# Optimization experiments

Measured on AMD Instinct MI355X. Metric: run time of the kernel, lower is better.

The kernel has to match this reference:

```python
import jax, jax.numpy as jnp
from jax import lax
import numpy as np

DIM = 512; DEPTH = 2; DSTATE = 16; EXPAND = 4; NEXP = 4
DIN = DIM * EXPAND; DTRANK = (DIM + 15) // 16; DCONV = 4; HID = DIM * EXPAND
BATCH = 2; SEQ = 2048; CAP_FACTOR = 1.0; EPS = 1e-6


def setup_inputs():
    key = jax.random.key(0)
    ks = jax.random.split(key, 12)
    f = lambda k, s: jax.random.normal(k, s, jnp.float32) * 0.02
    return {
        "x": jax.random.normal(ks[0], (BATCH, SEQ, DIM), jnp.float32),
        "in_w": f(ks[1], (DEPTH, 2 * DIN, DIM)),
        "conv_w": f(ks[2], (DEPTH, DIN, 1, DCONV)),
        "conv_b": jnp.zeros((DEPTH, DIN), jnp.float32),
        "xproj_w": f(ks[3], (DEPTH, DTRANK + 2 * DSTATE, DIN)),
        "dt_w": f(ks[4], (DEPTH, DIN, DTRANK)),
        "dt_b": jnp.zeros((DEPTH, DIN), jnp.float32),
        "A_log": jnp.tile(jnp.log(jnp.arange(1, DSTATE + 1, dtype=jnp.float32))[None, None, :], (DEPTH, DIN, 1)),
        "Dp": jnp.ones((DEPTH, DIN), jnp.float32),
        "out_w": f(ks[5], (DEPTH, DIM, DIN)),
        "gate_w": f(ks[6], (DEPTH, NEXP, DIM)),
        "gate_b": jnp.zeros((DEPTH, NEXP), jnp.float32),
        "w1": f(ks[7], (DEPTH, NEXP, HID, DIM)),
        "b1": jnp.zeros((DEPTH, NEXP, HID), jnp.float32),
        "w2": f(ks[8], (DEPTH, NEXP, DIM, HID)),
        "b2": jnp.zeros((DEPTH, NEXP, DIM), jnp.float32),
    }


def _switch_moe(x, gw, gb, w1, b1, w2, b2):
    # zeta SwitchGate: softmax -> top-1 mask -> normalize by batch-dim sum, scale by capacity
    gs = jax.nn.softmax(jnp.einsum('bld,ed->ble', x, gw) + gb, axis=-1)  # (b,l,E)
    mask = jax.nn.one_hot(jnp.argmax(gs, axis=-1), NEXP, dtype=gs.dtype)
    masked = gs * mask
    capacity = int(CAP_FACTOR * x.shape[0])
    gate = masked / (masked.sum(axis=0, keepdims=True) + EPS) * capacity  # (b,l,E)
    # zeta SwitchMoE runs every expert on every token, then gate-weighted sum
    h = jax.nn.gelu(jnp.einsum('bld,ehd->bleh', x, w1) + b1, approximate=False)  # (b,l,E,HID)
    eo = jnp.einsum('bleh,edh->bled', h, w2) + b2                                 # (b,l,E,d)
    return jnp.einsum('bled,ble->bld', eo, gate)


def _mamba(x, in_w, conv_w, conv_b, xproj_w, dt_w, dt_b, A_log, Dp, out_w):
    b, l, d = x.shape
    xz = jnp.einsum('bld,ed->ble', x, in_w)   # (b,l,2*DIN)
    u, res = xz[..., :DIN], xz[..., DIN:]
    # causal depthwise conv: torch pads both sides by DCONV-1 then crops to L == left-pad only
    uc = lax.conv_general_dilated(u.transpose(0, 2, 1), conv_w, (1,), [(DCONV - 1, 0)],
                                  feature_group_count=DIN,
                                  dimension_numbers=('NCH', 'OIH', 'NCH'))
    u = jax.nn.silu((uc + conv_b[None, :, None]).transpose(0, 2, 1))  # (b,l,DIN)
    dbc = jnp.einsum('bld,ed->ble', u, xproj_w)                       # (b,l,DTRANK+2n)
    delta = jax.nn.softplus(jnp.einsum('blr,dr->bld', dbc[..., :DTRANK], dt_w) + dt_b)  # (b,l,DIN)
    B = dbc[..., DTRANK:DTRANK + DSTATE]
    C = dbc[..., DTRANK + DSTATE:]
    A = -jnp.exp(A_log)                                               # (DIN,n)

    def step(s, t):
        dt, Bt, Ct, ut = t  # (b,DIN),(b,n),(b,n),(b,DIN)
        s = jnp.exp(dt[:, :, None] * A) * s + (dt * ut)[:, :, None] * Bt[:, None, :]
        return s, jnp.einsum('bdn,bn->bd', s, Ct)

    s0 = jnp.zeros((b, DIN, DSTATE), x.dtype)
    _, ys = lax.scan(step, s0, (delta.transpose(1, 0, 2), B.transpose(1, 0, 2),
                                C.transpose(1, 0, 2), u.transpose(1, 0, 2)))
    y = ys.transpose(1, 0, 2) + u * Dp
    y = y * jax.nn.silu(res)
    return jnp.einsum('ble,de->bld', y, out_w)


def reference(x, in_w, conv_w, conv_b, xproj_w, dt_w, dt_b, A_log, Dp, out_w,
              gate_w, gate_b, w1, b1, w2, b2):
    for i in range(DEPTH):
        x = _switch_moe(x, gate_w[i], gate_b[i], w1[i], b1[i], w2[i], b2[i])
        x = _mamba(x, in_w[i], conv_w[i], conv_b[i], xproj_w[i], dt_w[i], dt_b[i],
                   A_log[i], Dp[i], out_w[i]) + x
        x = _switch_moe(x, gate_w[i], gate_b[i], w1[i], b1[i], w2[i], b2[i])
    return x
```

## Files before the change

kernel.cpp:

```cpp
#include <hip/hip_runtime.h>
#include <math.h>
#include <stdint.h>

typedef unsigned short u16;
typedef __attribute__((ext_vector_type(8))) _Float16 f16x8;
typedef __attribute__((ext_vector_type(4))) float f32x4;
typedef __attribute__((ext_vector_type(4))) u16 u16x4;

constexpr int DIM_    = 512;
constexpr int NEXP_   = 4;
constexpr int DIN_    = 2048;
constexpr int DTRANK_ = 32;
constexpr int DSTATE_ = 16;
constexpr int HID_    = 2048;
constexpr int BATCH_  = 2;
constexpr int SEQ_    = 2048;
constexpr int NTOK_   = BATCH_ * SEQ_;
constexpr float EPS_  = 1e-6f;

constexpr int NCHUNK_ = 32;
constexpr int CLEN_   = SEQ_ / NCHUNK_;

__device__ __forceinline__ float siluf(float x)     { return x / (1.f + __expf(-x)); }
__device__ __forceinline__ float geluf(float x)     { return 0.5f * x * (1.f + erff(x * 0.70710678118654752440f)); }
__device__ __forceinline__ float softplusf(float x) { return x > 20.f ? x : log1pf(__expf(x)); }

__device__ __forceinline__ float h2f(u16 b) { return (float)__builtin_bit_cast(_Float16, b); }
__device__ __forceinline__ void fsplit(float v, u16& h, u16& l) {
    _Float16 hh = (_Float16)v;
    float r = v - (float)hh;
    _Float16 ll = (_Float16)r;
    h = __builtin_bit_cast(u16, hh);
    l = __builtin_bit_cast(u16, ll);
}

__device__ __forceinline__ void gload16(const void* g, void* l) {
    __builtin_amdgcn_global_load_lds(
        (const __attribute__((address_space(1))) unsigned*)(uintptr_t)g,
        (__attribute__((address_space(3))) unsigned*)(uintptr_t)l,
        16, 0, 0);
}

enum { EPI_NONE = 0, EPI_GELU = 1, EPI_SCALE_BIAS = 2, EPI_RESID = 4 };

template <int EPI, bool OUTF32, bool SPLITK = false>
__global__ __launch_bounds__(256, 2) void gemm_split(
    const u16* __restrict__ Ah, const u16* __restrict__ Al, int lda,
    const u16* __restrict__ Wh, const u16* __restrict__ Wl, int ldw, long wstride,
    const float* __restrict__ bias, int bstride,
    u16* __restrict__ Ch, u16* __restrict__ Cl, float* __restrict__ Cf, int ldc,
    int M, int K,
    const int* __restrict__ counts, const int* __restrict__ perm, int permstride,
    const float* __restrict__ scale,
    const u16* __restrict__ Rh, const u16* __restrict__ Rl, int ldr)
{
    const int nwg = gridDim.x * gridDim.y * gridDim.z;
    int lid = blockIdx.x + gridDim.x * (blockIdx.y + gridDim.y * blockIdx.z);
    {
        const int q = nwg >> 3, r = nwg & 7;
        const int xcd = lid & 7, idx = lid >> 3;
        lid = (xcd < r ? xcd * (q + 1) : r * (q + 1) + (xcd - r) * q) + idx;
    }
    const int bx = lid % gridDim.x;
    const int rest = lid / gridDim.x;
    const int by = rest % gridDim.y;
    const int bz = rest / gridDim.y;

    const int e  = (SPLITK || !counts) ? 0 : bz;
    const int Me = counts ? counts[e] : M;
    const int m0 = bx * 64;
    if (m0 >= Me) return;
    const int kbase = SPLITK ? bz * K : 0;
    const int n0 = by * 64;
    const int* rows = perm ? (perm + (long)e * permstride) : nullptr;
    const u16* Whe = Wh + (long)e * wstride;
    const u16* Wle = Wl + (long)e * wstride;
    const float* be = bias ? (bias + (long)e * bstride) : nullptr;
    float* Cfo = SPLITK ? (Cf + (size_t)bz * M * ldc) : Cf;

    __shared__ __attribute__((aligned(16))) u16 AsH[2][4096], AsL[2][4096];
    __shared__ __attribute__((aligned(16))) u16 BsH[2][4096], BsL[2][4096];

    const int tid  = threadIdx.x;
    const int lane = tid & 63;
    const int wave = tid >> 6;
    const int wr = wave >> 1, wc = wave & 1;

    const int slot = tid & 7;
    const int rloc = tid >> 3;
    const int eoff = ((slot ^ (rloc & 7)) << 3) + kbase;
    const int ldst = tid * 8;

    long asrc[2];
#pragma unroll
    for (int i = 0; i < 2; i++) {
        int gr = m0 + i * 32 + rloc;
        int src = rows ? rows[gr < Me ? gr : Me - 1] : gr;
        asrc[i] = (long)src * lda + eoff;
    }
    long bsrc[2];
#pragma unroll
    for (int i = 0; i < 2; i++)
        bsrc[i] = (long)(n0 + i * 32 + rloc) * ldw + eoff;

    auto stage = [&](int buf, int k0) {
#pragma unroll
        for (int i = 0; i < 2; i++) {
            gload16(Ah + asrc[i] + k0, &AsH[buf][i * 2048 + ldst]);
            gload16(Al + asrc[i] + k0, &AsL[buf][i * 2048 + ldst]);
            gload16(Whe + bsrc[i] + k0, &BsH[buf][i * 2048 + ldst]);
            gload16(Wle + bsrc[i] + k0, &BsL[buf][i * 2048 + ldst]);
        }
    };

    f32x4 zero = {0.f, 0.f, 0.f, 0.f};
    f32x4 acc[2][2];
#pragma unroll
    for (int m = 0; m < 2; m++)
#pragma unroll
        for (int n = 0; n < 2; n++) acc[m][n] = zero;

    const int lr = lane & 15;
    const int kq = (lane >> 4) * 8;

    const int NT = K / 64;
    stage(0, 0);
    __syncthreads();

    for (int t = 0; t < NT; ++t) {
        const int buf = t & 1;
        if (t + 1 < NT) stage(buf ^ 1, (t + 1) * 64);
#pragma unroll
        for (int kk = 0; kk < 2; kk++) {
            const int lk = kk * 32 + kq;
            f16x8 ah[2], al[2], bh[2], bl[2];
#pragma unroll
            for (int m = 0; m < 2; m++) {
                int row = wr * 32 + m * 16 + lr;
                int off = row * 64 + (lk ^ ((row & 7) << 3));
                ah[m] = *(const f16x8*)&AsH[buf][off];
                al[m] = *(const f16x8*)&AsL[buf][off];
            }
#pragma unroll
            for (int n = 0; n < 2; n++) {
                int row = wc * 32 + n * 16 + lr;
                int off = row * 64 + (lk ^ ((row & 7) << 3));
                bh[n] = *(const f16x8*)&BsH[buf][off];
                bl[n] = *(const f16x8*)&BsL[buf][off];
            }
#pragma unroll
            for (int m = 0; m < 2; m++)
#pragma unroll
                for (int n = 0; n < 2; n++) {
                    acc[m][n] = __builtin_amdgcn_mfma_f32_16x16x32_f16(ah[m], bh[n], acc[m][n], 0, 0, 0);
                    acc[m][n] = __builtin_amdgcn_mfma_f32_16x16x32_f16(ah[m], bl[n], acc[m][n], 0, 0, 0);
                    acc[m][n] = __builtin_amdgcn_mfma_f32_16x16x32_f16(al[m], bh[n], acc[m][n], 0, 0, 0);
                }
        }
        __syncthreads();
    }

    const int rq = lane >> 4;
#pragma unroll
    for (int m = 0; m < 2; m++) {
#pragma unroll
        for (int n = 0; n < 2; n++) {
            const int col = n0 + wc * 32 + n * 16 + lr;
            const float bv = be ? be[col] : 0.f;
#pragma unroll
            for (int r = 0; r < 4; r++) {
                const int gr = m0 + wr * 32 + m * 16 + rq * 4 + r;
                if (gr >= Me) continue;
                const long crow = rows ? rows[gr] : gr;
                float v = acc[m][n][r];
                if constexpr (EPI == EPI_GELU)            v = geluf(v + bv);
                else if constexpr (EPI == EPI_SCALE_BIAS) v = scale[crow] * (v + bv);
                else if constexpr (EPI == EPI_RESID)
                    v += h2f(Rh[crow * ldr + col]) + h2f(Rl[crow * ldr + col]);
                if constexpr (OUTF32) {
                    Cfo[crow * ldc + col] = v;
                } else {
                    u16 hh, ll; fsplit(v, hh, ll);
                    Ch[crow * ldc + col] = hh;
                    Cl[crow * ldc + col] = ll;
                }
            }
        }
    }
}

__global__ __launch_bounds__(256) void sum4_kernel(
    const float* __restrict__ p, float* __restrict__ out, int n)
{
    int i = (blockIdx.x * 256 + threadIdx.x) * 4;
    if (i >= n) return;
    float4 a = *(const float4*)(p + i);
    float4 b = *(const float4*)(p + n + i);
    float4 c = *(const float4*)(p + 2 * (size_t)n + i);
    float4 d = *(const float4*)(p + 3 * (size_t)n + i);
    float4 o = make_float4(a.x + b.x + c.x + d.x, a.y + b.y + c.y + d.y,
                           a.z + b.z + c.z + d.z, a.w + b.w + c.w + d.w);
    *(float4*)(out + i) = o;
}

__global__ __launch_bounds__(256) void cvt_split(
    const float* __restrict__ in, u16* __restrict__ oh, u16* __restrict__ ol, int n)
{
    int i = (blockIdx.x * 256 + threadIdx.x) * 4;
    if (i >= n) return;
    float4 v = *(const float4*)(in + i);
    u16 h0, l0, h1, l1, h2, l2, h3, l3;
    fsplit(v.x, h0, l0); fsplit(v.y, h1, l1);
    fsplit(v.z, h2, l2); fsplit(v.w, h3, l3);
    u16x4 hv = {h0, h1, h2, h3}, lv = {l0, l1, l2, l3};
    *(u16x4*)(oh + i) = hv;
    *(u16x4*)(ol + i) = lv;
}

__global__ __launch_bounds__(128) void gate_kernel(
    const u16* __restrict__ Xh, const u16* __restrict__ Xl,
    const float* __restrict__ gw, const float* __restrict__ gb,
    float* __restrict__ gval, int* __restrict__ perm, int* __restrict__ counts)
{
    const int l    = blockIdx.x;
    const int wv   = threadIdx.x >> 6;
    const int lane = threadIdx.x & 63;
    const int t    = wv * SEQ_ + l;
    const size_t xb = (size_t)t * DIM_;
    float a0 = 0, a1 = 0, a2 = 0, a3 = 0;
    for (int k = lane; k < DIM_; k += 64) {
        float xv = h2f(Xh[xb + k]) + h2f(Xl[xb + k]);
        a0 += xv * gw[0 * DIM_ + k];
        a1 += xv * gw[1 * DIM_ + k];
        a2 += xv * gw[2 * DIM_ + k];
        a3 += xv * gw[3 * DIM_ + k];
    }
#pragma unroll
    for (int off = 32; off; off >>= 1) {
        a0 += __shfl_xor(a0, off);
        a1 += __shfl_xor(a1, off);
        a2 += __shfl_xor(a2, off);
        a3 += __shfl_xor(a3, off);
    }
    __shared__ float sval[2];
    __shared__ int   sidx[2];
    if (lane == 0) {
        float lg[4] = { a0 + gb[0], a1 + gb[1], a2 + gb[2], a3 + gb[3] };
        int bi = 0; float m = lg[0];
#pragma unroll
        for (int q = 1; q < 4; q++) if (lg[q] > m) { m = lg[q]; bi = q; }
        float s = 0.f;
#pragma unroll
        for (int q = 0; q < 4; q++) s += __expf(lg[q] - m);
        sval[wv] = 1.f / s;
        sidx[wv] = bi;
    }
    __syncthreads();
    if (lane == 0) {
        float myv = sval[wv]; int myi = sidx[wv];
        float ov  = sval[wv ^ 1]; int oi = sidx[wv ^ 1];
        float denom = myv + (oi == myi ? ov : 0.f) + EPS_;
        gval[t] = myv / denom * 2.0f;
        int pos = atomicAdd(&counts[myi], 1);
        perm[myi * NTOK_ + pos] = t;
    }
}

__global__ __launch_bounds__(256) void conv_silu_kernel(
    const float* __restrict__ xz, const float* __restrict__ cw,
    const float* __restrict__ cb, u16* __restrict__ Uh, u16* __restrict__ Ul)
{
    const long idx = (long)blockIdx.x * blockDim.x + threadIdx.x;
    const int c = (int)(idx & (DIN_ - 1));
    const int t = (int)(idx >> 11);
    const int l = t & (SEQ_ - 1);
    const float* base = xz + (size_t)t * (2 * DIN_) + c;
    float w0 = cw[c * 4 + 0], w1 = cw[c * 4 + 1], w2 = cw[c * 4 + 2], w3 = cw[c * 4 + 3];
    float acc = cb[c] + w3 * base[0];
    if (l >= 1) acc += w2 * base[-1L * (2 * DIN_)];
    if (l >= 2) acc += w1 * base[-2L * (2 * DIN_)];
    if (l >= 3) acc += w0 * base[-3L * (2 * DIN_)];
    float u = siluf(acc);
    u16 h, lo; fsplit(u, h, lo);
    Uh[idx] = h; Ul[idx] = lo;
}

__global__ __launch_bounds__(256) void gemm_dt(
    const float* __restrict__ A,
    const float* __restrict__ W,
    const float* __restrict__ bias,
    float* __restrict__ C)
{
    const int m0 = blockIdx.x * 64;
    const int n0 = blockIdx.y * 64;
    __shared__ float As[16][65];
    __shared__ float Bs[16][65];
    const int tid  = threadIdx.x;
    const int lrow = tid >> 2;
    const int lk4  = (tid & 3) << 2;
    const int tx   = tid & 15, ty = tid >> 4;
    const float* Aptr = A + (long)(m0 + lrow) * 64 + lk4;
    const float* Wptr = W + (long)(n0 + lrow) * 32 + lk4;
    float acc[4][4] = {};
    for (int k0 = 0; k0 < 32; k0 += 16) {
        float4 av = *(const float4*)(Aptr + k0);
        float4 wv = *(const float4*)(Wptr + k0);
        As[lk4 + 0][lrow] = av.x; As[lk4 + 1][lrow] = av.y;
        As[lk4 + 2][lrow] = av.z; As[lk4 + 3][lrow] = av.w;
        Bs[lk4 + 0][lrow] = wv.x; Bs[lk4 + 1][lrow] = wv.y;
        Bs[lk4 + 2][lrow] = wv.z; Bs[lk4 + 3][lrow] = wv.w;
        __syncthreads();
#pragma unroll
        for (int k = 0; k < 16; k++) {
            float a0 = As[k][ty * 4 + 0], a1 = As[k][ty * 4 + 1],
                  a2 = As[k][ty * 4 + 2], a3 = As[k][ty * 4 + 3];
            float b0 = Bs[k][tx * 4 + 0], b1 = Bs[k][tx * 4 + 1],
                  b2 = Bs[k][tx * 4 + 2], b3 = Bs[k][tx * 4 + 3];
            acc[0][0] += a0 * b0; acc[0][1] += a0 * b1; acc[0][2] += a0 * b2; acc[0][3] += a0 * b3;
            acc[1][0] += a1 * b0; acc[1][1] += a1 * b1; acc[1][2] += a1 * b2; acc[1][3] += a1 * b3;
            acc[2][0] += a2 * b0; acc[2][1] += a2 * b1; acc[2][2] += a2 * b2; acc[2][3] += a2 * b3;
            acc[3][0] += a3 * b0; acc[3][1] += a3 * b1; acc[3][2] += a3 * b2; acc[3][3] += a3 * b3;
        }
        __syncthreads();
    }
#pragma unroll
    for (int i = 0; i < 4; i++) {
        float4 out;
#pragma unroll
        for (int j = 0; j < 4; j++)
            (&out.x)[j] = softplusf(acc[i][j] + bias[n0 + tx * 4 + j]);
        *(float4*)(C + (long)(m0 + ty * 4 + i) * DIN_ + n0 + tx * 4) = out;
    }
}

__global__ __launch_bounds__(256) void scan_part(
    const float* __restrict__ delta,
    const u16* __restrict__ Uh, const u16* __restrict__ Ul,
    const float* __restrict__ dbc, const float* __restrict__ A_log,
    float* __restrict__ sloc, float* __restrict__ sdt)
{
    const int d = blockIdx.x * 256 + threadIdx.x;
    const int c = blockIdx.y;
    const int b = blockIdx.z;
    float Ad[DSTATE_];
#pragma unroll
    for (int n = 0; n < DSTATE_; n++) Ad[n] = -__expf(A_log[d * DSTATE_ + n]);
    float s[DSTATE_];
#pragma unroll
    for (int n = 0; n < DSTATE_; n++) s[n] = 0.f;
    float sumdt = 0.f;
    const int tbase = b * SEQ_ + c * CLEN_;
    for (int l = 0; l < CLEN_; l++) {
        const size_t idx = (size_t)(tbase + l) * DIN_ + d;
        const float dt = delta[idx];
        const float uu = h2f(Uh[idx]) + h2f(Ul[idx]);
        const float du = dt * uu;
        sumdt += dt;
        const float* bc = dbc + (size_t)(tbase + l) * 64;
#pragma unroll
        for (int n = 0; n < DSTATE_; n++)
            s[n] = __expf(dt * Ad[n]) * s[n] + du * bc[32 + n];
    }
    const int bc_ = b * NCHUNK_ + c;
#pragma unroll
    for (int n = 0; n < DSTATE_; n++)
        sloc[((size_t)bc_ * DSTATE_ + n) * DIN_ + d] = s[n];
    sdt[(size_t)bc_ * DIN_ + d] = sumdt;
}

__global__ __launch_bounds__(256) void scan_combine(
    float* __restrict__ sloc, const float* __restrict__ sdt,
    const float* __restrict__ A_log)
{
    const int id = blockIdx.x * 256 + threadIdx.x;
    const int d  = id & (DIN_ - 1);
    const int rest = id >> 11;
    const int n  = rest & (DSTATE_ - 1);
    const int b  = rest >> 4;
    const float Ad = -__expf(A_log[d * DSTATE_ + n]);
    float sin = 0.f;
    for (int c = 0; c < NCHUNK_; c++) {
        const int bc_ = b * NCHUNK_ + c;
        const size_t idx = ((size_t)bc_ * DSTATE_ + n) * DIN_ + d;
        const float slocal = sloc[idx];
        const float P = __expf(sdt[(size_t)bc_ * DIN_ + d] * Ad);
        sloc[idx] = sin;
        sin = P * sin + slocal;
    }
}

__global__ __launch_bounds__(256) void scan_final(
    const float* __restrict__ delta,
    u16* Uh, u16* Ul,
    const float* __restrict__ dbc, const float* __restrict__ A_log,
    const float* __restrict__ Dp, const float* __restrict__ xz,
    const float* __restrict__ sloc)
{
    const int d = blockIdx.x * 256 + threadIdx.x;
    const int c = blockIdx.y;
    const int b = blockIdx.z;
    float Ad[DSTATE_];
#pragma unroll
    for (int n = 0; n < DSTATE_; n++) Ad[n] = -__expf(A_log[d * DSTATE_ + n]);
    const float Dd = Dp[d];
    const int bc_ = b * NCHUNK_ + c;
    float s[DSTATE_];
#pragma unroll
    for (int n = 0; n < DSTATE_; n++)
        s[n] = sloc[((size_t)bc_ * DSTATE_ + n) * DIN_ + d];
    const int tbase = b * SEQ_ + c * CLEN_;
    for (int l = 0; l < CLEN_; l++) {
        const int t = tbase + l;
        const size_t idx = (size_t)t * DIN_ + d;
        const float dt = delta[idx];
        const float uu = h2f(Uh[idx]) + h2f(Ul[idx]);
        const float du = dt * uu;
        const float* bc = dbc + (size_t)t * 64;
        float sum = 0.f;
#pragma unroll
        for (int n = 0; n < DSTATE_; n++) {
            float sn = __expf(dt * Ad[n]) * s[n] + du * bc[32 + n];
            s[n] = sn;
            sum += sn * bc[48 + n];
        }
        const float res = xz[(size_t)t * (2 * DIN_) + DIN_ + d];
        float y = (sum + uu * Dd) * siluf(res);
        u16 hh, ll; fsplit(y, hh, ll);
        Uh[idx] = hh; Ul[idx] = ll;
    }
}

extern "C" void kernel_launch(void* const* d_in, const int* in_sizes, int n_in,
                              void* d_out, int out_size, void* d_ws, size_t ws_size,
                              hipStream_t stream)
{
    const float* x0      = (const float*)d_in[0];
    const float* in_w    = (const float*)d_in[1];
    const float* conv_w  = (const float*)d_in[2];
    const float* conv_b  = (const float*)d_in[3];
    const float* xproj_w = (const float*)d_in[4];
    const float* dt_w    = (const float*)d_in[5];
    const float* dt_b    = (const float*)d_in[6];
    const float* A_log   = (const float*)d_in[7];
    const float* Dp      = (const float*)d_in[8];
    const float* out_w   = (const float*)d_in[9];
    const float* gate_w  = (const float*)d_in[10];
    const float* gate_b  = (const float*)d_in[11];
    const float* w1      = (const float*)d_in[12];
    const float* b1      = (const float*)d_in[13];
    const float* w2      = (const float*)d_in[14];
    const float* b2      = (const float*)d_in[15];

    char* p = (char*)d_ws;
    auto carve = [&](size_t bytes) -> void* {
        void* r = (void*)p;
        p += (bytes + 255) & ~(size_t)255;
        return r;
    };
    const size_t NX = (size_t)NTOK_ * DIM_;
    const size_t NU = (size_t)NTOK_ * DIN_;
    u16* XaH = (u16*)carve(NX * 2); u16* XaL = (u16*)carve(NX * 2);
    u16* XbH = (u16*)carve(NX * 2); u16* XbL = (u16*)carve(NX * 2);
    float* xz    = (float*)carve((size_t)NTOK_ * 2 * DIN_ * 4);
    u16* UH  = (u16*)carve(NU * 2);
    u16* UL  = (u16*)carve(NU * 2);
    float* delta = (float*)carve(NU * 4);
    float* dbc   = (float*)carve((size_t)NTOK_ * 64 * 4);
    float* xpp   = (float*)carve((size_t)4 * NTOK_ * 64 * 4);
    float* sloc  = (float*)carve((size_t)BATCH_ * NCHUNK_ * DSTATE_ * DIN_ * 4);
    float* sdt   = (float*)carve((size_t)BATCH_ * NCHUNK_ * DIN_ * 4);
    float* gval  = (float*)carve((size_t)NTOK_ * 4);
    int*   perm  = (int*)carve((size_t)NEXP_ * NTOK_ * 4);
    int*   counts = (int*)carve(256);
    const size_t NW1 = (size_t)NEXP_ * HID_ * DIM_;
    u16* w1H = (u16*)carve(NW1 * 2); u16* w1L = (u16*)carve(NW1 * 2);
    u16* w2H = (u16*)carve(NW1 * 2); u16* w2L = (u16*)carve(NW1 * 2);
    const size_t NIW = (size_t)2 * DIN_ * DIM_;
    u16* iwH = (u16*)carve(NIW * 2); u16* iwL = (u16*)carve(NIW * 2);
    const size_t NOW = (size_t)DIM_ * DIN_;
    u16* owH = (u16*)carve(NOW * 2); u16* owL = (u16*)carve(NOW * 2);
    const size_t NXP = (size_t)64 * DIN_;
    u16* xpH = (u16*)carve(NXP * 2); u16* xpL = (u16*)carve(NXP * 2);

    auto cvt = [&](const float* in, u16* oh, u16* ol, size_t n) {
        cvt_split<<<(unsigned)((n / 4 + 255) / 256), 256, 0, stream>>>(in, oh, ol, (int)n);
    };

    auto moe = [&](const u16* Xh, const u16* Xl, u16* Oh, u16* Ol, float* Of, int dep) {
        hipMemsetAsync(counts, 0, NEXP_ * sizeof(int), stream);
        gate_kernel<<<SEQ_, 128, 0, stream>>>(
            Xh, Xl, gate_w + (size_t)dep * NEXP_ * DIM_, gate_b + dep * NEXP_,
            gval, perm, counts);
        gemm_split<EPI_GELU, false><<<dim3(NTOK_ / 64, HID_ / 64, NEXP_), 256, 0, stream>>>(
            Xh, Xl, DIM_, w1H, w1L, DIM_, (long)HID_ * DIM_,
            b1 + (size_t)dep * NEXP_ * HID_, HID_,
            UH, UL, nullptr, HID_, NTOK_, DIM_,
            counts, perm, NTOK_, nullptr, nullptr, nullptr, 0);
        if (Of) {
            gemm_split<EPI_SCALE_BIAS, true><<<dim3(NTOK_ / 64, DIM_ / 64, NEXP_), 256, 0, stream>>>(
                UH, UL, HID_, w2H, w2L, HID_, (long)DIM_ * HID_,
                b2 + (size_t)dep * NEXP_ * DIM_, DIM_,
                nullptr, nullptr, Of, DIM_, NTOK_, HID_,
                counts, perm, NTOK_, gval, nullptr, nullptr, 0);
        } else {
            gemm_split<EPI_SCALE_BIAS, false><<<dim3(NTOK_ / 64, DIM_ / 64, NEXP_), 256, 0, stream>>>(
                UH, UL, HID_, w2H, w2L, HID_, (long)DIM_ * HID_,
                b2 + (size_t)dep * NEXP_ * DIM_, DIM_,
                Oh, Ol, nullptr, DIM_, NTOK_, HID_,
                counts, perm, NTOK_, gval, nullptr, nullptr, 0);
        }
    };

    auto mamba = [&](const u16* Xh, const u16* Xl, u16* Oh, u16* Ol, int dep) {
        gemm_split<EPI_NONE, true><<<dim3(NTOK_ / 64, (2 * DIN_) / 64, 1), 256, 0, stream>>>(
            Xh, Xl, DIM_, iwH, iwL, DIM_, 0, nullptr, 0,
            nullptr, nullptr, xz, 2 * DIN_, NTOK_, DIM_,
            nullptr, nullptr, 0, nullptr, nullptr, nullptr, 0);
        conv_silu_kernel<<<(NTOK_ * DIN_) / 256, 256, 0, stream>>>(
            xz, conv_w + (size_t)dep * DIN_ * 4, conv_b + dep * DIN_, UH, UL);
        gemm_split<EPI_NONE, true, true><<<dim3(NTOK_ / 64, 1, 4), 256, 0, stream>>>(
            UH, UL, DIN_, xpH, xpL, DIN_, 0, nullptr, 0,
            nullptr, nullptr, xpp, 64, NTOK_, DIN_ / 4,
            nullptr, nullptr, 0, nullptr, nullptr, nullptr, 0);
        sum4_kernel<<<(NTOK_ * 64) / 1024, 256, 0, stream>>>(xpp, dbc, NTOK_ * 64);
        gemm_dt<<<dim3(NTOK_ / 64, DIN_ / 64), 256, 0, stream>>>(
            dbc, dt_w + (size_t)dep * DIN_ * DTRANK_, dt_b + dep * DIN_, delta);
        const float* Al = A_log + (size_t)dep * DIN_ * DSTATE_;
        scan_part<<<dim3(DIN_ / 256, NCHUNK_, BATCH_), 256, 0, stream>>>(
            delta, UH, UL, dbc, Al, sloc, sdt);
        scan_combine<<<(BATCH_ * DSTATE_ * DIN_) / 256, 256, 0, stream>>>(sloc, sdt, Al);
        scan_final<<<dim3(DIN_ / 256, NCHUNK_, BATCH_), 256, 0, stream>>>(
            delta, UH, UL, dbc, Al, Dp + dep * DIN_, xz, sloc);
        gemm_split<EPI_RESID, false><<<dim3(NTOK_ / 64, DIM_ / 64, 1), 256, 0, stream>>>(
            UH, UL, DIN_, owH, owL, DIN_, 0, nullptr, 0,
            Oh, Ol, nullptr, DIM_, NTOK_, DIN_,
            nullptr, nullptr, 0, nullptr, Xh, Xl, DIM_);
    };

    cvt(x0, XaH, XaL, NX);
    for (int dep = 0; dep < 2; dep++) {
        cvt(in_w + (size_t)dep * NIW, iwH, iwL, NIW);
        cvt(xproj_w + (size_t)dep * NXP, xpH, xpL, NXP);
        cvt(out_w + (size_t)dep * NOW, owH, owL, NOW);
        cvt(w1 + (size_t)dep * NW1, w1H, w1L, NW1);
        cvt(w2 + (size_t)dep * NW1, w2H, w2L, NW1);
        if (dep == 0) {
            moe(XaH, XaL, XbH, XbL, nullptr, 0);
            mamba(XbH, XbL, XaH, XaL, 0);
            moe(XaH, XaL, XbH, XbL, nullptr, 0);
        } else {
            moe(XbH, XbL, XaH, XaL, nullptr, 1);
            mamba(XaH, XaL, XbH, XbL, 1);
            moe(XbH, XbL, nullptr, nullptr, (float*)d_out, 1);
        }
    }
}
```

Measured before the change: 1.527 ms.

## Use 512-thread blocks with 8 waves per 64x64 GEMM tile, drop XCD remap

The split-fp16 GEMM now runs 8 waves per 64x64 output tile instead of 4. Each wave computes a 32x16 sub-tile (2 MFMA accumulators instead of 4), and each thread stages one 16-byte chunk per buffer instead of two. The XCD-aware block-index remapping is removed in favor of plain blockIdx ordering. The goal is more waves in flight to hide LDS and global latency. The cost is less register-level reuse of A fragments per B fragment, more LDS reads per MFMA, and possibly worse L2 locality across XCDs.

```diff
diff --git a/kernel.cpp b/kernel.cpp
--- a/kernel.cpp
+++ b/kernel.cpp
@@ -44,7 +44,7 @@
 enum { EPI_NONE = 0, EPI_GELU = 1, EPI_SCALE_BIAS = 2, EPI_RESID = 4 };
 
 template <int EPI, bool OUTF32, bool SPLITK = false>
-__global__ __launch_bounds__(256, 2) void gemm_split(
+__global__ __launch_bounds__(512, 4) void gemm_split(
     const u16* __restrict__ Ah, const u16* __restrict__ Al, int lda,
     const u16* __restrict__ Wh, const u16* __restrict__ Wl, int ldw, long wstride,
     const float* __restrict__ bias, int bstride,
@@ -54,17 +54,7 @@
     const float* __restrict__ scale,
     const u16* __restrict__ Rh, const u16* __restrict__ Rl, int ldr)
 {
-    const int nwg = gridDim.x * gridDim.y * gridDim.z;
-    int lid = blockIdx.x + gridDim.x * (blockIdx.y + gridDim.y * blockIdx.z);
-    {
-        const int q = nwg >> 3, r = nwg & 7;
-        const int xcd = lid & 7, idx = lid >> 3;
-        lid = (xcd < r ? xcd * (q + 1) : r * (q + 1) + (xcd - r) * q) + idx;
-    }
-    const int bx = lid % gridDim.x;
-    const int rest = lid / gridDim.x;
-    const int by = rest % gridDim.y;
-    const int bz = rest / gridDim.y;
+    const int bx = blockIdx.x, by = blockIdx.y, bz = blockIdx.z;
 
     const int e  = (SPLITK || !counts) ? 0 : bz;
     const int Me = counts ? counts[e] : M;
@@ -84,41 +74,31 @@
     const int tid  = threadIdx.x;
     const int lane = tid & 63;
     const int wave = tid >> 6;
-    const int wr = wave >> 1, wc = wave & 1;
+    const int wr = wave >> 2, wc = wave & 3;
 
     const int slot = tid & 7;
     const int rloc = tid >> 3;
     const int eoff = ((slot ^ (rloc & 7)) << 3) + kbase;
     const int ldst = tid * 8;
 
-    long asrc[2];
-#pragma unroll
-    for (int i = 0; i < 2; i++) {
-        int gr = m0 + i * 32 + rloc;
+    long asrc;
+    {
+        int gr = m0 + rloc;
         int src = rows ? rows[gr < Me ? gr : Me - 1] : gr;
-        asrc[i] = (long)src * lda + eoff;
-    }
-    long bsrc[2];
-#pragma unroll
-    for (int i = 0; i < 2; i++)
-        bsrc[i] = (long)(n0 + i * 32 + rloc) * ldw + eoff;
+        asrc = (long)src * lda + eoff;
+    }
+    const long bsrc = (long)(n0 + rloc) * ldw + eoff;
 
     auto stage = [&](int buf, int k0) {
-#pragma unroll
-        for (int i = 0; i < 2; i++) {
-            gload16(Ah + asrc[i] + k0, &AsH[buf][i * 2048 + ldst]);
-            gload16(Al + asrc[i] + k0, &AsL[buf][i * 2048 + ldst]);
-            gload16(Whe + bsrc[i] + k0, &BsH[buf][i * 2048 + ldst]);
-            gload16(Wle + bsrc[i] + k0, &BsL[buf][i * 2048 + ldst]);
-        }
+        gload16(Ah + asrc + k0, &AsH[buf][ldst]);
+        gload16(Al + asrc + k0, &AsL[buf][ldst]);
+        gload16(Whe + bsrc + k0, &BsH[buf][ldst]);
+        gload16(Wle + bsrc + k0, &BsL[buf][ldst]);
     };
 
     f32x4 zero = {0.f, 0.f, 0.f, 0.f};
-    f32x4 acc[2][2];
-#pragma unroll
-    for (int m = 0; m < 2; m++)
-#pragma unroll
-        for (int n = 0; n < 2; n++) acc[m][n] = zero;
+    f32x4 acc[2];
+    acc[0] = zero; acc[1] = zero;
 
     const int lr = lane & 15;
     const int kq = (lane >> 4) * 8;
@@ -133,7 +113,13 @@
 #pragma unroll
         for (int kk = 0; kk < 2; kk++) {
             const int lk = kk * 32 + kq;
-            f16x8 ah[2], al[2], bh[2], bl[2];
+            f16x8 ah[2], al[2], bh, bl;
+            {
+                int row = wc * 16 + lr;
+                int off = row * 64 + (lk ^ ((row & 7) << 3));
+                bh = *(const f16x8*)&BsH[buf][off];
+                bl = *(const f16x8*)&BsL[buf][off];
+            }
 #pragma unroll
             for (int m = 0; m < 2; m++) {
                 int row = wr * 32 + m * 16 + lr;
@@ -142,48 +128,36 @@
                 al[m] = *(const f16x8*)&AsL[buf][off];
             }
 #pragma unroll
-            for (int n = 0; n < 2; n++) {
-                int row = wc * 32 + n * 16 + lr;
-                int off = row * 64 + (lk ^ ((row & 7) << 3));
-                bh[n] = *(const f16x8*)&BsH[buf][off];
-                bl[n] = *(const f16x8*)&BsL[buf][off];
+            for (int m = 0; m < 2; m++) {
+                acc[m] = __builtin_amdgcn_mfma_f32_16x16x32_f16(ah[m], bh, acc[m], 0, 0, 0);
+                acc[m] = __builtin_amdgcn_mfma_f32_16x16x32_f16(ah[m], bl, acc[m], 0, 0, 0);
+                acc[m] = __builtin_amdgcn_mfma_f32_16x16x32_f16(al[m], bh, acc[m], 0, 0, 0);
             }
-#pragma unroll
-            for (int m = 0; m < 2; m++)
-#pragma unroll
-                for (int n = 0; n < 2; n++) {
-                    acc[m][n] = __builtin_amdgcn_mfma_f32_16x16x32_f16(ah[m], bh[n], acc[m][n], 0, 0, 0);
-                    acc[m][n] = __builtin_amdgcn_mfma_f32_16x16x32_f16(ah[m], bl[n], acc[m][n], 0, 0, 0);
-                    acc[m][n] = __builtin_amdgcn_mfma_f32_16x16x32_f16(al[m], bh[n], acc[m][n], 0, 0, 0);
-                }
         }
         __syncthreads();
     }
 
     const int rq = lane >> 4;
+    const int col = n0 + wc * 16 + lr;
+    const float bv = be ? be[col] : 0.f;
 #pragma unroll
     for (int m = 0; m < 2; m++) {
 #pragma unroll
-        for (int n = 0; n < 2; n++) {
-            const int col = n0 + wc * 32 + n * 16 + lr;
-            const float bv = be ? be[col] : 0.f;
-#pragma unroll
-            for (int r = 0; r < 4; r++) {
-                const int gr = m0 + wr * 32 + m * 16 + rq * 4 + r;
-                if (gr >= Me) continue;
-                const long crow = rows ? rows[gr] : gr;
-                float v = acc[m][n][r];
-                if constexpr (EPI == EPI_GELU)            v = geluf(v + bv);
-                else if constexpr (EPI == EPI_SCALE_BIAS) v = scale[crow] * (v + bv);
-                else if constexpr (EPI == EPI_RESID)
-                    v += h2f(Rh[crow * ldr + col]) + h2f(Rl[crow * ldr + col]);
-                if constexpr (OUTF32) {
-                    Cfo[crow * ldc + col] = v;
-                } else {
-                    u16 hh, ll; fsplit(v, hh, ll);
-                    Ch[crow * ldc + col] = hh;
-                    Cl[crow * ldc + col] = ll;
-                }
+        for (int r = 0; r < 4; r++) {
+            const int gr = m0 + wr * 32 + m * 16 + rq * 4 + r;
+            if (gr >= Me) continue;
+            const long crow = rows ? rows[gr] : gr;
+            float v = acc[m][r];
+            if constexpr (EPI == EPI_GELU)            v = geluf(v + bv);
+            else if constexpr (EPI == EPI_SCALE_BIAS) v = scale[crow] * (v + bv);
+            else if constexpr (EPI == EPI_RESID)
+                v += h2f(Rh[crow * ldr + col]) + h2f(Rl[crow * ldr + col]);
+            if constexpr (OUTF32) {
+                Cfo[crow * ldc + col] = v;
+            } else {
+                u16 hh, ll; fsplit(v, hh, ll);
+                Ch[crow * ldc + col] = hh;
+                Cl[crow * ldc + col] = ll;
             }
         }
     }
@@ -491,19 +465,19 @@
         gate_kernel<<<SEQ_, 128, 0, stream>>>(
             Xh, Xl, gate_w + (size_t)dep * NEXP_ * DIM_, gate_b + dep * NEXP_,
             gval, perm, counts);
-        gemm_split<EPI_GELU, false><<<dim3(NTOK_ / 64, HID_ / 64, NEXP_), 256, 0, stream>>>(
+        gemm_split<EPI_GELU, false><<<dim3(NTOK_ / 64, HID_ / 64, NEXP_), 512, 0, stream>>>(
             Xh, Xl, DIM_, w1H, w1L, DIM_, (long)HID_ * DIM_,
             b1 + (size_t)dep * NEXP_ * HID_, HID_,
             UH, UL, nullptr, HID_, NTOK_, DIM_,
             counts, perm, NTOK_, nullptr, nullptr, nullptr, 0);
         if (Of) {
-            gemm_split<EPI_SCALE_BIAS, true><<<dim3(NTOK_ / 64, DIM_ / 64, NEXP_), 256, 0, stream>>>(
+            gemm_split<EPI_SCALE_BIAS, true><<<dim3(NTOK_ / 64, DIM_ / 64, NEXP_), 512, 0, stream>>>(
                 UH, UL, HID_, w2H, w2L, HID_, (long)DIM_ * HID_,
                 b2 + (size_t)dep * NEXP_ * DIM_, DIM_,
                 nullptr, nullptr, Of, DIM_, NTOK_, HID_,
                 counts, perm, NTOK_, gval, nullptr, nullptr, 0);
         } else {
-            gemm_split<EPI_SCALE_BIAS, false><<<dim3(NTOK_ / 64, DIM_ / 64, NEXP_), 256, 0, stream>>>(
+            gemm_split<EPI_SCALE_BIAS, false><<<dim3(NTOK_ / 64, DIM_ / 64, NEXP_), 512, 0, stream>>>(
                 UH, UL, HID_, w2H, w2L, HID_, (long)DIM_ * HID_,
                 b2 + (size_t)dep * NEXP_ * DIM_, DIM_,
                 Oh, Ol, nullptr, DIM_, NTOK_, HID_,
@@ -512,13 +486,13 @@
     };
 
     auto mamba = [&](const u16* Xh, const u16* Xl, u16* Oh, u16* Ol, int dep) {
-        gemm_split<EPI_NONE, true><<<dim3(NTOK_ / 64, (2 * DIN_) / 64, 1), 256, 0, stream>>>(
+        gemm_split<EPI_NONE, true><<<dim3(NTOK_ / 64, (2 * DIN_) / 64, 1), 512, 0, stream>>>(
             Xh, Xl, DIM_, iwH, iwL, DIM_, 0, nullptr, 0,
             nullptr, nullptr, xz, 2 * DIN_, NTOK_, DIM_,
             nullptr, nullptr, 0, nullptr, nullptr, nullptr, 0);
         conv_silu_kernel<<<(NTOK_ * DIN_) / 256, 256, 0, stream>>>(
             xz, conv_w + (size_t)dep * DIN_ * 4, conv_b + dep * DIN_, UH, UL);
-        gemm_split<EPI_NONE, true, true><<<dim3(NTOK_ / 64, 1, 4), 256, 0, stream>>>(
+        gemm_split<EPI_NONE, true, true><<<dim3(NTOK_ / 64, 1, 4), 512, 0, stream>>>(
             UH, UL, DIN_, xpH, xpL, DIN_, 0, nullptr, 0,
             nullptr, nullptr, xpp, 64, NTOK_, DIN_ / 4,
             nullptr, nullptr, 0, nullptr, nullptr, nullptr, 0);
@@ -531,7 +505,7 @@
         scan_combine<<<(BATCH_ * DSTATE_ * DIN_) / 256, 256, 0, stream>>>(sloc, sdt, Al);
         scan_final<<<dim3(DIN_ / 256, NCHUNK_, BATCH_), 256, 0, stream>>>(
             delta, UH, UL, dbc, Al, Dp + dep * DIN_, xz, sloc);
-        gemm_split<EPI_RESID, false><<<dim3(NTOK_ / 64, DIM_ / 64, 1), 256, 0, stream>>>(
+        gemm_split<EPI_RESID, false><<<dim3(NTOK_ / 64, DIM_ / 64, 1), 512, 0, stream>>>(
             UH, UL, DIN_, owH, owL, DIN_, 0, nullptr, 0,
             Oh, Ol, nullptr, DIM_, NTOK_, DIN_,
             nullptr, nullptr, 0, nullptr, Xh, Xl, DIM_);
```

Measured after the change: 1.533 ms. About the same (+0.4%).
